# Optimization experiments

Hardware: AMD Instinct MI355X
Metric: run time of the kernel (lower is better)

The kernel has to match this reference:

```python
import jax, jax.numpy as jnp
import numpy as np

D_MODEL = 512
N_HEADS = 8
D_HEAD = D_MODEL // N_HEADS


def entmax15(z, axis=-1):
    """Exact sort-based entmax-1.5 along `axis` (Peters et al. 2019)."""
    z = jnp.moveaxis(z, axis, -1)
    x = z / 2.0
    x = x - jnp.max(x, axis=-1, keepdims=True)
    x_srt = -jnp.sort(-x, axis=-1)  # descending
    D = x_srt.shape[-1]
    k = jnp.arange(1, D + 1, dtype=x.dtype)
    cs = jnp.cumsum(x_srt, axis=-1)
    cs2 = jnp.cumsum(x_srt * x_srt, axis=-1)
    mean = cs / k
    ss = k * (cs2 / k - mean * mean)
    delta = (1.0 - ss) / k
    tau = mean - jnp.sqrt(jnp.clip(delta, 0.0))
    support = (tau <= x_srt).astype(jnp.int32)
    support_size = jnp.sum(support, axis=-1, keepdims=True)  # >= 1
    tau_star = jnp.take_along_axis(tau, support_size - 1, axis=-1)
    out = jnp.square(jnp.clip(x - tau_star, 0.0))
    return jnp.moveaxis(out, -1, axis)


def setup_inputs() -> dict:
    key = jax.random.key(0)
    ks = jax.random.split(key, 12)
    B, L = 8, 1024
    s = 1.0 / np.sqrt(D_MODEL)
    inp = {
        "query": jax.random.normal(ks[0], (B, L, D_MODEL), jnp.float32),
        "key": jax.random.normal(ks[1], (B, L, D_MODEL), jnp.float32),
        "value": jax.random.normal(ks[2], (B, L, D_MODEL), jnp.float32),
        "key_padding_mask": jnp.zeros((B, L), jnp.bool_),
        "q_w": jax.random.uniform(ks[3], (D_MODEL, D_MODEL), jnp.float32, -s, s),
        "q_b": jax.random.uniform(ks[4], (D_MODEL,), jnp.float32, -s, s),
        "k_w": jax.random.uniform(ks[5], (D_MODEL, D_MODEL), jnp.float32, -s, s),
        "k_b": jax.random.uniform(ks[6], (D_MODEL,), jnp.float32, -s, s),
        "v_w": jax.random.uniform(ks[7], (D_MODEL, D_MODEL), jnp.float32, -s, s),
        "v_b": jax.random.uniform(ks[8], (D_MODEL,), jnp.float32, -s, s),
        "out_w": jax.random.uniform(ks[9], (D_MODEL, D_MODEL), jnp.float32, -s, s),
        "out_b": jax.random.uniform(ks[10], (D_MODEL,), jnp.float32, -s, s),
    }
    return inp


def reference(query, key, value, key_padding_mask, q_w, q_b, k_w, k_b, v_w, v_b, out_w, out_b):
    B, L, _ = query.shape
    scale = D_HEAD ** -0.5
    # torch Linear: y = x @ W^T + b
    def split_heads(x):
        return x.reshape(B, L, N_HEADS, D_HEAD).transpose(0, 2, 1, 3)  # [B,H,L,d]
    q = split_heads(query @ q_w.T + q_b)
    k = split_heads(key @ k_w.T + k_b)
    v = split_heads(value @ v_w.T + v_b)
    scores = jnp.einsum('bhqd,bhkd->bhqk', q, k) * scale  # [B,H,L,L]
    mask = key_padding_mask[:, None, None, :]
    scores = jnp.where(mask, jnp.asarray(-1e9, scores.dtype), scores)
    attn = entmax15(scores, axis=-1)  # dropout in eval mode -> identity
    ctx = jnp.einsum('bhqk,bhkd->bhqd', attn, v)
    ctx = ctx.transpose(0, 2, 1, 3).reshape(B, L, D_MODEL)
    return ctx @ out_w.T + out_b
```

## Files before the change

### kernel.cpp

```cpp
#include <hip/hip_runtime.h>
#include <stdint.h>

typedef _Float16 f16;
typedef __attribute__((ext_vector_type(8))) f16 f16x8;
typedef __attribute__((ext_vector_type(2))) f16 h2;
typedef __attribute__((ext_vector_type(4))) float f32x4;
typedef unsigned short u16;
typedef unsigned int u32;
typedef unsigned char u8;

#define LL 1024
#define DM 512

__device__ __forceinline__ u16 f2h(float f){ return __builtin_bit_cast(u16, (f16)f); }
__device__ __forceinline__ u32 pack2(float a, float b){
  h2 v; v.x = (f16)a; v.y = (f16)b; return __builtin_bit_cast(u32, v);
}
__device__ __forceinline__ f32x4 mfma16h(f16x8 a, f16x8 b, f32x4 c){
  return __builtin_amdgcn_mfma_f32_16x16x32_f16(a, b, c, 0, 0, 0);
}

template<int CTRL>
__device__ __forceinline__ float dpp_mov(float x){
  return __builtin_bit_cast(float,
    __builtin_amdgcn_update_dpp(0, __builtin_bit_cast(int, x), CTRL, 0xF, 0xF, true));
}
__device__ __forceinline__ float red_add16(float v){
  v += dpp_mov<0x128>(v);
  v += dpp_mov<0x124>(v);
  v += dpp_mov<0x122>(v);
  v += dpp_mov<0x121>(v);
  return v;
}
__device__ __forceinline__ float red_max16(float v){
  v = fmaxf(v, dpp_mov<0x128>(v));
  v = fmaxf(v, dpp_mov<0x124>(v));
  v = fmaxf(v, dpp_mov<0x122>(v));
  v = fmaxf(v, dpp_mov<0x121>(v));
  return v;
}
__device__ __forceinline__ float red_add32(float v){
  v = red_add16(v);
  v += __shfl_xor(v, 16);
  return v;
}
__device__ __forceinline__ float red_max32(float v){
  v = red_max16(v);
  v = fmaxf(v, __shfl_xor(v, 16));
  return v;
}

struct CvtArgs {
  const float* src[7];
  u16* dst[7];
  int n4[7];
};

__global__ __launch_bounds__(256) void cvt_kernel(CvtArgs a){
  int seg = blockIdx.y;
  const float4* s = (const float4*)a.src[seg];
  ushort4* d = (ushort4*)a.dst[seg];
  int n4 = a.n4[seg];
  for (int i = blockIdx.x*blockDim.x + threadIdx.x; i < n4; i += gridDim.x*blockDim.x){
    float4 v = s[i];
    ushort4 o;
    o.x = f2h(v.x); o.y = f2h(v.y); o.z = f2h(v.z); o.w = f2h(v.w);
    d[i] = o;
  }
}

struct QkvArgs {
  const u16* A[3];
  const u16* W[3];
  const float* bias[3];
  u16* dst[3];
  float scale[3];
};

__global__ __launch_bounds__(256,2) void proj_qkv(QkvArgs args){
  __shared__ u16 SM[128*128];
  u16* As = SM;
  u16* Bs = SM + 128*64;
  const int tid = threadIdx.x;
  const int w = tid>>6, lane = tid&63;
  const int g = lane>>4, r16 = lane&15;
  const int wr = w>>1, wc = w&1;

  const int which = blockIdx.y>>2, nt = blockIdx.y&3;
  const bool isV = (which==2);
  const u16* A = args.A[which];
  const u16* W = args.W[which];
  const float* bias = args.bias[which];
  u16* dsth = args.dst[which];
  const float scale = args.scale[which];

  const int m0 = blockIdx.x*128, n0 = nt*128;

  f32x4 acc[4][4] = {};

  int rowc[4], slc[4];
  #pragma unroll
  for (int i=0;i<4;++i){
    int c = i*256+tid;
    rowc[i] = c>>3;
    slc[i] = (c&7) ^ ((c>>3)&7);
  }

  const int fswz = r16 & 7;

  for (int k0=0; k0<DM; k0+=64){
    #pragma unroll
    for (int i=0;i<4;++i){
      int c = i*256+tid;
      __builtin_amdgcn_global_load_lds(
        (const __attribute__((address_space(1))) void*)(A + (size_t)(m0+rowc[i])*DM + k0 + slc[i]*8),
        (__attribute__((address_space(3))) void*)(&As[c*8]), 16, 0, 0);
      __builtin_amdgcn_global_load_lds(
        (const __attribute__((address_space(1))) void*)(W + (size_t)(n0+rowc[i])*DM + k0 + slc[i]*8),
        (__attribute__((address_space(3))) void*)(&Bs[c*8]), 16, 0, 0);
    }
    __syncthreads();

    f16x8 af[4][2], bfr[4][2];
    #pragma unroll
    for (int mi=0; mi<4; ++mi){
      int row = wr*64 + mi*16 + r16;
      #pragma unroll
      for (int ks=0; ks<2; ++ks)
        af[mi][ks] = *(const f16x8*)(&As[row*64 + ((ks*4+g)^fswz)*8]);
    }
    #pragma unroll
    for (int ni=0; ni<4; ++ni){
      int row = wc*64 + ni*16 + r16;
      #pragma unroll
      for (int ks=0; ks<2; ++ks)
        bfr[ni][ks] = *(const f16x8*)(&Bs[row*64 + ((ks*4+g)^fswz)*8]);
    }
    if (isV){
      #pragma unroll
      for (int mi=0; mi<4; ++mi)
        #pragma unroll
        for (int ni=0; ni<4; ++ni){
          acc[mi][ni] = mfma16h(af[mi][0], bfr[ni][0], acc[mi][ni]);
          acc[mi][ni] = mfma16h(af[mi][1], bfr[ni][1], acc[mi][ni]);
        }
    } else {
      #pragma unroll
      for (int mi=0; mi<4; ++mi)
        #pragma unroll
        for (int ni=0; ni<4; ++ni){
          acc[mi][ni] = mfma16h(bfr[ni][0], af[mi][0], acc[mi][ni]);
          acc[mi][ni] = mfma16h(bfr[ni][1], af[mi][1], acc[mi][ni]);
        }
    }
    __syncthreads();
  }

  if (!isV){
    #pragma unroll
    for (int mi=0; mi<4; ++mi){
      #pragma unroll
      for (int ni=0; ni<4; ++ni){
        f32x4 a = acc[mi][ni];
        int row = wr*64 + mi*16 + r16;
        int c   = wc*16 + ni*4 + g;
        float4 bv = *(const float4*)(bias + n0 + c*4);
        uint2 pk;
        pk.x = pack2((a[0]+bv.x)*scale, (a[1]+bv.y)*scale);
        pk.y = pack2((a[2]+bv.z)*scale, (a[3]+bv.w)*scale);
        *(uint2*)(&SM[row*128 + ((c ^ ((row&7)<<2))<<2)]) = pk;
      }
    }
  } else {
    #pragma unroll
    for (int mi=0; mi<4; ++mi){
      #pragma unroll
      for (int ni=0; ni<4; ++ni){
        f32x4 a = acc[mi][ni];
        int fl = wc*64 + ni*16 + r16;
        int kc = wr*16 + mi*4 + g;
        float bv = bias[n0 + fl];
        uint2 pk;
        pk.x = pack2(a[0]+bv, a[1]+bv);
        pk.y = pack2(a[2]+bv, a[3]+bv);
        *(uint2*)(&SM[fl*128 + ((kc ^ ((fl&7)<<2))<<2)]) = pk;
      }
    }
  }
  __syncthreads();

  #pragma unroll
  for (int rr=0; rr<8; ++rr){
    int row = w*32 + rr*4 + (lane>>4);
    int c0 = (lane&15)*2;
    int cs = c0 ^ ((row&7)<<2);
    uint4 v = *(const uint4*)(&SM[row*128 + (cs<<2)]);
    if (!isV){
      *(uint4*)(dsth + (size_t)(m0+row)*DM + n0 + (c0<<2)) = v;
    } else {
      int n = n0 + row;
      int hh = n>>6, d = n&63, bb = m0>>10;
      *(uint4*)(dsth + (size_t)((bb*8+hh)*64 + d)*1024 + (m0&1023) + (c0<<2)) = v;
    }
  }
}

__global__ __launch_bounds__(256,2) void proj_out(
    const u16* __restrict__ A, const u16* __restrict__ W,
    const float* __restrict__ bias, float* __restrict__ dstf)
{
  __shared__ u16 As[64*64];
  __shared__ u16 Bs[128*64];
  const int tid = threadIdx.x;
  const int w = tid>>6, lane = tid&63;
  const int g = lane>>4, r16 = lane&15;
  const int m0 = blockIdx.x*64, n0 = blockIdx.y*128;

  f32x4 acc[4][2] = {};

  int rowa[2], slota[2];
  #pragma unroll
  for (int i=0;i<2;++i){ int c = i*256+tid; rowa[i]=c>>3; slota[i]=c&7; }
  int rowb[4], slotb[4];
  #pragma unroll
  for (int i=0;i<4;++i){ int c = i*256+tid; rowb[i]=c>>3; slotb[i]=c&7; }

  uint4 ra[2], rb[4];
  #pragma unroll
  for (int i=0;i<2;++i)
    ra[i] = *(const uint4*)(A + (size_t)(m0+rowa[i])*DM + slota[i]*8);
  #pragma unroll
  for (int i=0;i<4;++i)
    rb[i] = *(const uint4*)(W + (size_t)(n0+rowb[i])*DM + slotb[i]*8);

  const int fswz = r16 & 7;

  for (int k0=0; k0<DM; k0+=64){
    __syncthreads();
    #pragma unroll
    for (int i=0;i<2;++i)
      *(uint4*)(&As[rowa[i]*64 + (slota[i]^(rowa[i]&7))*8]) = ra[i];
    #pragma unroll
    for (int i=0;i<4;++i)
      *(uint4*)(&Bs[rowb[i]*64 + (slotb[i]^(rowb[i]&7))*8]) = rb[i];
    __syncthreads();
    int kn = (k0+64 < DM) ? (k0+64) : 0;
    #pragma unroll
    for (int i=0;i<2;++i)
      ra[i] = *(const uint4*)(A + (size_t)(m0+rowa[i])*DM + kn + slota[i]*8);
    #pragma unroll
    for (int i=0;i<4;++i)
      rb[i] = *(const uint4*)(W + (size_t)(n0+rowb[i])*DM + kn + slotb[i]*8);

    f16x8 af[4][2], bfr[2][2];
    #pragma unroll
    for (int mi=0; mi<4; ++mi){
      int row = mi*16 + r16;
      #pragma unroll
      for (int ks=0; ks<2; ++ks)
        af[mi][ks] = *(const f16x8*)(&As[row*64 + ((ks*4+g)^fswz)*8]);
    }
    #pragma unroll
    for (int ni=0; ni<2; ++ni){
      int row = w*32 + ni*16 + r16;
      #pragma unroll
      for (int ks=0; ks<2; ++ks)
        bfr[ni][ks] = *(const f16x8*)(&Bs[row*64 + ((ks*4+g)^fswz)*8]);
    }
    #pragma unroll
    for (int mi=0; mi<4; ++mi)
      #pragma unroll
      for (int ni=0; ni<2; ++ni){
        acc[mi][ni] = mfma16h(bfr[ni][0], af[mi][0], acc[mi][ni]);
        acc[mi][ni] = mfma16h(bfr[ni][1], af[mi][1], acc[mi][ni]);
      }
  }

  #pragma unroll
  for (int mi=0; mi<4; ++mi){
    #pragma unroll
    for (int ni=0; ni<2; ++ni){
      int m  = m0 + mi*16 + r16;
      int nb = n0 + w*32 + ni*16 + g*4;
      float4 bv = *(const float4*)(bias + nb);
      float4 o;
      o.x = acc[mi][ni][0]+bv.x; o.y = acc[mi][ni][1]+bv.y;
      o.z = acc[mi][ni][2]+bv.z; o.w = acc[mi][ni][3]+bv.w;
      *(float4*)(dstf + (size_t)m*DM + nb) = o;
    }
  }
}

__global__ __launch_bounds__(1024,8) void attn_entmax(
    const u16* __restrict__ Qf, const u16* __restrict__ Kf,
    const u16* __restrict__ Vt, const u8* __restrict__ mask,
    u16* __restrict__ ctx)
{
  __shared__ u16 S[32*1024];
  __shared__ float P2[2048];

  const int tid = threadIdx.x, w = tid>>6, lane = tid&63;
  const int g = lane>>4, r16 = lane&15;
  const int bid = blockIdx.x;
  const int bh = ((bid&7)<<3) | ((bid>>3)&7);
  const int qb = bid>>6;
  const int b = bh>>3, h = bh&7;
  const int q0 = qb*32;
  const u16* Qb = Qf + ((size_t)(b*LL + q0))*DM + h*64;
  const u16* Kb = Kf + ((size_t)(b*LL))*DM + h*64;

  f16x8 qf[2][2];
  #pragma unroll
  for (int qi=0;qi<2;++qi){
    qf[qi][0] = *(const f16x8*)(Qb + (size_t)(qi*16 + r16)*DM + g*8);
    qf[qi][1] = *(const f16x8*)(Qb + (size_t)(qi*16 + r16)*DM + 32 + g*8);
  }
  {
    f16x8 kc0, kc1, kn0, kn1;
    {
      const u16* kp = Kb + (size_t)(w*64 + r16)*DM + g*8;
      kc0 = *(const f16x8*)(kp);
      kc1 = *(const f16x8*)(kp + 32);
    }
    #pragma unroll
    for (int kt=0; kt<4; ++kt){
      if (kt < 3){
        const u16* kp = Kb + (size_t)(w*64 + (kt+1)*16 + r16)*DM + g*8;
        kn0 = *(const f16x8*)(kp);
        kn1 = *(const f16x8*)(kp + 32);
      }
      int kb = w*64 + kt*16 + g*4;
      u32 m4 = *(const u32*)(mask + b*LL + kb);
      #pragma unroll
      for (int qi=0; qi<2; ++qi){
        f32x4 acc = {};
        acc = mfma16h(kc0, qf[qi][0], acc);
        acc = mfma16h(kc1, qf[qi][1], acc);
        float v0 = (m4 & 0xFFu)       ? -30000.f : acc[0];
        float v1 = (m4 & 0xFF00u)     ? -30000.f : acc[1];
        float v2 = (m4 & 0xFF0000u)   ? -30000.f : acc[2];
        float v3 = (m4 & 0xFF000000u) ? -30000.f : acc[3];
        int row = qi*16 + r16;
        int cc = ((kb>>6)&7) ^ (row&7);
        uint2 pk; pk.x = pack2(v0,v1); pk.y = pack2(v2,v3);
        *(uint2*)(&S[row*LL + (kb ^ (cc<<3))]) = pk;
      }
      kc0 = kn0; kc1 = kn1;
    }
  }
  __syncthreads();

  {
    const int row = w*2 + (lane>>5);
    const int l32 = lane&31;
    int offs[4];
    h2 zp[16];
    #pragma unroll
    for (int c=0;c<4;++c){
      int kb = l32*32 + c*8;
      int cc = ((kb>>6)&7) ^ (row&7);
      offs[c] = row*LL + (kb ^ (cc<<3));
      uint4 v = *(const uint4*)(&S[offs[c]]);
      zp[c*4+0] = __builtin_bit_cast(h2, v.x);
      zp[c*4+1] = __builtin_bit_cast(h2, v.y);
      zp[c*4+2] = __builtin_bit_cast(h2, v.z);
      zp[c*4+3] = __builtin_bit_cast(h2, v.w);
    }
    h2 m2 = zp[0];
    #pragma unroll
    for (int t=1;t<16;++t) m2 = __builtin_elementwise_max(m2, zp[t]);
    float mx = red_max32(fmaxf((float)m2.x, (float)m2.y));

    const h2 zero2 = (h2)(f16)0;
    float lo = mx - 1.0f, hi = mx, tau = mx - 0.5f;
    #pragma unroll 1
    for (int it=0; it<6; ++it){
      f16 th = (f16)tau;
      h2 t2; t2.x = th; t2.y = th;
      h2 s1a = zero2, s1b = zero2, s2a = zero2, s2b = zero2;
      #pragma unroll
      for (int t=0;t<16;t+=2){
        h2 d0 = __builtin_elementwise_max(zp[t]   - t2, zero2);
        h2 d1 = __builtin_elementwise_max(zp[t+1] - t2, zero2);
        s1a = s1a + d0;        s1b = s1b + d1;
        s2a = s2a + d0*d0;     s2b = s2b + d1*d1;
      }
      h2 s1h = s1a + s1b, s2h = s2a + s2b;
      float s1 = red_add32((float)s1h.x + (float)s1h.y);
      float s2 = red_add32((float)s2h.x + (float)s2h.y);
      if (s2 >= 1.0f) lo = tau; else hi = tau;
      float tn = tau + (s2 - 1.0f)/(2.0f*s1);
      tau = (tn >= lo && tn < hi) ? tn : 0.5f*(lo+hi);
    }

    {
      f16 th = (f16)tau;
      h2 t2; t2.x = th; t2.y = th;
      h2 psa = zero2, psb = zero2;
      #pragma unroll
      for (int t=0;t<16;t+=2){
        h2 d0 = __builtin_elementwise_max(zp[t]   - t2, zero2);
        h2 d1 = __builtin_elementwise_max(zp[t+1] - t2, zero2);
        h2 p0 = d0*d0, p1 = d1*d1;
        zp[t] = p0; zp[t+1] = p1;
        psa = psa + p0; psb = psb + p1;
      }
      h2 ps2 = psa + psb;
      float ps = red_add32((float)ps2.x + (float)ps2.y);
      f16 iv = (f16)(1.0f/ps);
      h2 i2; i2.x = iv; i2.y = iv;
      #pragma unroll
      for (int c=0;c<4;++c){
        uint4 v;
        v.x = __builtin_bit_cast(u32, (h2)(zp[c*4+0]*i2));
        v.y = __builtin_bit_cast(u32, (h2)(zp[c*4+1]*i2));
        v.z = __builtin_bit_cast(u32, (h2)(zp[c*4+2]*i2));
        v.w = __builtin_bit_cast(u32, (h2)(zp[c*4+3]*i2));
        *(uint4*)(&S[offs[c]]) = v;
      }
    }
  }
  __syncthreads();

  const int qi = w>>3, di = (w>>1)&3, kh = w&1;
  const u16* vrow = Vt + (size_t)(bh*64 + di*16 + r16)*LL;
  const int prow = qi*16 + r16;
  f32x4 o0 = {}, o1 = {};
  {
    f16x8 pc0, pc1, vc0, vc1, pn0, pn1, vn0, vn1;
    const int base = kh*16;
    {
      int k0c = (base+0)*32 + g*8;
      int k1c = (base+1)*32 + g*8;
      int cc0 = ((k0c>>6)&7) ^ (prow&7);
      int cc1 = ((k1c>>6)&7) ^ (prow&7);
      pc0 = *(const f16x8*)(&S[prow*LL + (k0c ^ (cc0<<3))]);
      vc0 = *(const f16x8*)(vrow + k0c);
      pc1 = *(const f16x8*)(&S[prow*LL + (k1c ^ (cc1<<3))]);
      vc1 = *(const f16x8*)(vrow + k1c);
    }
    #pragma unroll
    for (int grp=0; grp<8; ++grp){
      if (grp < 7){
        int k0n = (base+grp*2+2)*32 + g*8;
        int k1n = (base+grp*2+3)*32 + g*8;
        int cc0 = ((k0n>>6)&7) ^ (prow&7);
        int cc1 = ((k1n>>6)&7) ^ (prow&7);
        pn0 = *(const f16x8*)(&S[prow*LL + (k0n ^ (cc0<<3))]);
        vn0 = *(const f16x8*)(vrow + k0n);
        pn1 = *(const f16x8*)(&S[prow*LL + (k1n ^ (cc1<<3))]);
        vn1 = *(const f16x8*)(vrow + k1n);
      }
      o0 = mfma16h(pc0, vc0, o0);
      o1 = mfma16h(pc1, vc1, o1);
      pc0 = pn0; vc0 = vn0; pc1 = pn1; vc1 = vn1;
    }
  }
  const int pair = qi*4 + di;
  if (kh == 1){
    float4 o;
    o.x = o0[0]+o1[0]; o.y = o0[1]+o1[1]; o.z = o0[2]+o1[2]; o.w = o0[3]+o1[3];
    *(float4*)(&P2[pair*256 + r16*16 + g*4]) = o;
  }
  __syncthreads();
  if (kh == 0){
    float4 p = *(const float4*)(&P2[pair*256 + r16*16 + g*4]);
    u16* cp = ctx + (size_t)(b*LL + q0 + qi*16 + g*4)*DM + h*64 + di*16 + r16;
    cp[0*DM] = f2h(o0[0]+o1[0]+p.x);
    cp[1*DM] = f2h(o0[1]+o1[1]+p.y);
    cp[2*DM] = f2h(o0[2]+o1[2]+p.z);
    cp[3*DM] = f2h(o0[3]+o1[3]+p.w);
  }
}

extern "C" void kernel_launch(void* const* d_in, const int* in_sizes, int n_in,
                              void* d_out, int out_size, void* d_ws, size_t ws_size,
                              hipStream_t stream) {
  const float* query = (const float*)d_in[0];
  const float* key   = (const float*)d_in[1];
  const float* value = (const float*)d_in[2];
  const u8*    maskp = (const u8*)d_in[3];
  const float* q_w = (const float*)d_in[4];
  const float* q_b = (const float*)d_in[5];
  const float* k_w = (const float*)d_in[6];
  const float* k_b = (const float*)d_in[7];
  const float* v_w = (const float*)d_in[8];
  const float* v_b = (const float*)d_in[9];
  const float* out_w = (const float*)d_in[10];
  const float* out_b = (const float*)d_in[11];
  float* out = (float*)d_out;

  u16* qx = (u16*)d_ws;
  u16* kx = qx + 4194304;
  u16* vx = kx + 4194304;
  u16* wq = vx + 4194304;
  u16* wk = wq + 262144;
  u16* wv = wk + 262144;
  u16* wo = wv + 262144;
  u16* Qbuf = wo + 262144;
  u16* Kbuf = Qbuf + 4194304;
  u16* Vt   = Kbuf + 4194304;
  u16* ctxb = Vt + 4194304;

  CvtArgs ca;
  ca.src[0]=query; ca.dst[0]=qx; ca.n4[0]=8*LL*DM/4;
  ca.src[1]=key;   ca.dst[1]=kx; ca.n4[1]=8*LL*DM/4;
  ca.src[2]=value; ca.dst[2]=vx; ca.n4[2]=8*LL*DM/4;
  ca.src[3]=q_w;   ca.dst[3]=wq; ca.n4[3]=DM*DM/4;
  ca.src[4]=k_w;   ca.dst[4]=wk; ca.n4[4]=DM*DM/4;
  ca.src[5]=v_w;   ca.dst[5]=wv; ca.n4[5]=DM*DM/4;
  ca.src[6]=out_w; ca.dst[6]=wo; ca.n4[6]=DM*DM/4;
  cvt_kernel<<<dim3(512,7),256,0,stream>>>(ca);

  QkvArgs qa;
  qa.A[0]=qx; qa.A[1]=kx; qa.A[2]=vx;
  qa.W[0]=wq; qa.W[1]=wk; qa.W[2]=wv;
  qa.bias[0]=q_b; qa.bias[1]=k_b; qa.bias[2]=v_b;
  qa.dst[0]=Qbuf; qa.dst[1]=Kbuf; qa.dst[2]=Vt;
  qa.scale[0]=0.0625f; qa.scale[1]=1.0f; qa.scale[2]=1.0f;

  proj_qkv<<<dim3(64,12),256,0,stream>>>(qa);

  attn_entmax<<<dim3(2048),1024,0,stream>>>(Qbuf, Kbuf, Vt, maskp, ctxb);

  proj_out<<<dim3(128,4),256,0,stream>>>(ctxb, wo, out_b, out);
}
```

Measured before the change: 186.2 us.

## Halve attention block to 8 waves and software-pipeline QK/entmax/PV over two row halves

The attention kernel now runs 512 threads instead of 1024 and splits its 32 query rows into two 16-row halves. Score computation, entmax normalisation and the PV matmul are staggered across the halves, with odd and even waves doing the phases in opposite order so MFMA work and VALU/reduction work from different waves can overlap. s_setprio is raised around the PV MFMA loop, and the split-K partial buffer is double-buffered so the first half's output store overlaps the second half's PV. Each wave now does twice the work, and the kernel adds an extra barrier and changes occupancy through the new launch bounds.

```diff
diff --git a/kernel.cpp b/kernel.cpp
--- a/kernel.cpp
+++ b/kernel.cpp
@@ -291,13 +291,14 @@
   }
 }
 
-__global__ __launch_bounds__(1024,8) void attn_entmax(
+__global__ __launch_bounds__(512,4) void attn_entmax(
     const u16* __restrict__ Qf, const u16* __restrict__ Kf,
     const u16* __restrict__ Vt, const u8* __restrict__ mask,
     u16* __restrict__ ctx)
 {
   __shared__ u16 S[32*1024];
-  __shared__ float P2[2048];
+  __shared__ float P2a[1024];
+  __shared__ float P2b[1024];
 
   const int tid = threadIdx.x, w = tid>>6, lane = tid&63;
   const int g = lane>>4, r16 = lane&15;
@@ -308,6 +309,7 @@
   const int q0 = qb*32;
   const u16* Qb = Qf + ((size_t)(b*LL + q0))*DM + h*64;
   const u16* Kb = Kf + ((size_t)(b*LL))*DM + h*64;
+  const int di = w&3, kh = w>>2;
 
   f16x8 qf[2][2];
   #pragma unroll
@@ -315,43 +317,32 @@
     qf[qi][0] = *(const f16x8*)(Qb + (size_t)(qi*16 + r16)*DM + g*8);
     qf[qi][1] = *(const f16x8*)(Qb + (size_t)(qi*16 + r16)*DM + 32 + g*8);
   }
-  {
-    f16x8 kc0, kc1, kn0, kn1;
-    {
-      const u16* kp = Kb + (size_t)(w*64 + r16)*DM + g*8;
-      kc0 = *(const f16x8*)(kp);
-      kc1 = *(const f16x8*)(kp + 32);
-    }
-    #pragma unroll
-    for (int kt=0; kt<4; ++kt){
-      if (kt < 3){
-        const u16* kp = Kb + (size_t)(w*64 + (kt+1)*16 + r16)*DM + g*8;
-        kn0 = *(const f16x8*)(kp);
-        kn1 = *(const f16x8*)(kp + 32);
-      }
-      int kb = w*64 + kt*16 + g*4;
+
+  auto phaseA = [&](int hf){
+    #pragma unroll
+    for (int kt=0; kt<8; ++kt){
+      int krow = w*128 + kt*16;
+      const u16* kp = Kb + (size_t)(krow + r16)*DM + g*8;
+      f16x8 kf0 = *(const f16x8*)(kp);
+      f16x8 kf1 = *(const f16x8*)(kp + 32);
+      int kb = krow + g*4;
       u32 m4 = *(const u32*)(mask + b*LL + kb);
-      #pragma unroll
-      for (int qi=0; qi<2; ++qi){
-        f32x4 acc = {};
-        acc = mfma16h(kc0, qf[qi][0], acc);
-        acc = mfma16h(kc1, qf[qi][1], acc);
-        float v0 = (m4 & 0xFFu)       ? -30000.f : acc[0];
-        float v1 = (m4 & 0xFF00u)     ? -30000.f : acc[1];
-        float v2 = (m4 & 0xFF0000u)   ? -30000.f : acc[2];
-        float v3 = (m4 & 0xFF000000u) ? -30000.f : acc[3];
-        int row = qi*16 + r16;
-        int cc = ((kb>>6)&7) ^ (row&7);
-        uint2 pk; pk.x = pack2(v0,v1); pk.y = pack2(v2,v3);
-        *(uint2*)(&S[row*LL + (kb ^ (cc<<3))]) = pk;
-      }
-      kc0 = kn0; kc1 = kn1;
-    }
-  }
-  __syncthreads();
-
-  {
-    const int row = w*2 + (lane>>5);
+      f32x4 acc = {};
+      acc = mfma16h(kf0, qf[hf][0], acc);
+      acc = mfma16h(kf1, qf[hf][1], acc);
+      float v0 = (m4 & 0xFFu)       ? -30000.f : acc[0];
+      float v1 = (m4 & 0xFF00u)     ? -30000.f : acc[1];
+      float v2 = (m4 & 0xFF0000u)   ? -30000.f : acc[2];
+      float v3 = (m4 & 0xFF000000u) ? -30000.f : acc[3];
+      int row = hf*16 + r16;
+      int cc = ((kb>>6)&7) ^ (row&7);
+      uint2 pk; pk.x = pack2(v0,v1); pk.y = pack2(v2,v3);
+      *(uint2*)(&S[row*LL + (kb ^ (cc<<3))]) = pk;
+    }
+  };
+
+  auto phaseB = [&](int hf){
+    const int row = hf*16 + w*2 + (lane>>5);
     const int l32 = lane&31;
     int offs[4];
     h2 zp[16];
@@ -392,7 +383,6 @@
       float tn = tau + (s2 - 1.0f)/(2.0f*s1);
       tau = (tn >= lo && tn < hi) ? tn : 0.5f*(lo+hi);
     }
-
     {
       f16 th = (f16)tau;
       h2 t2; t2.x = th; t2.y = th;
@@ -419,16 +409,13 @@
         *(uint4*)(&S[offs[c]]) = v;
       }
     }
-  }
-  __syncthreads();
-
-  const int qi = w>>3, di = (w>>1)&3, kh = w&1;
-  const u16* vrow = Vt + (size_t)(bh*64 + di*16 + r16)*LL;
-  const int prow = qi*16 + r16;
-  f32x4 o0 = {}, o1 = {};
-  {
+  };
+
+  auto phaseC = [&](int hf, f32x4& o0, f32x4& o1, float* P2x){
+    const u16* vrow = Vt + (size_t)(bh*64 + di*16 + r16)*LL;
+    const int prow = hf*16 + r16;
+    const int base = kh*16;
     f16x8 pc0, pc1, vc0, vc1, pn0, pn1, vn0, vn1;
-    const int base = kh*16;
     {
       int k0c = (base+0)*32 + g*8;
       int k1c = (base+1)*32 + g*8;
@@ -439,6 +426,7 @@
       pc1 = *(const f16x8*)(&S[prow*LL + (k1c ^ (cc1<<3))]);
       vc1 = *(const f16x8*)(vrow + k1c);
     }
+    __builtin_amdgcn_s_setprio(1);
     #pragma unroll
     for (int grp=0; grp<8; ++grp){
       if (grp < 7){
@@ -455,22 +443,41 @@
       o1 = mfma16h(pc1, vc1, o1);
       pc0 = pn0; vc0 = vn0; pc1 = pn1; vc1 = vn1;
     }
-  }
-  const int pair = qi*4 + di;
-  if (kh == 1){
-    float4 o;
-    o.x = o0[0]+o1[0]; o.y = o0[1]+o1[1]; o.z = o0[2]+o1[2]; o.w = o0[3]+o1[3];
-    *(float4*)(&P2[pair*256 + r16*16 + g*4]) = o;
-  }
-  __syncthreads();
-  if (kh == 0){
-    float4 p = *(const float4*)(&P2[pair*256 + r16*16 + g*4]);
-    u16* cp = ctx + (size_t)(b*LL + q0 + qi*16 + g*4)*DM + h*64 + di*16 + r16;
+    __builtin_amdgcn_s_setprio(0);
+    if (kh == 1){
+      float4 o;
+      o.x = o0[0]+o1[0]; o.y = o0[1]+o1[1]; o.z = o0[2]+o1[2]; o.w = o0[3]+o1[3];
+      *(float4*)(&P2x[di*256 + r16*16 + g*4]) = o;
+    }
+  };
+
+  auto mergeStore = [&](int hf, f32x4 o0, f32x4 o1, const float* P2x){
+    float4 p = *(const float4*)(&P2x[di*256 + r16*16 + g*4]);
+    u16* cp = ctx + (size_t)(b*LL + q0 + hf*16 + g*4)*DM + h*64 + di*16 + r16;
     cp[0*DM] = f2h(o0[0]+o1[0]+p.x);
     cp[1*DM] = f2h(o0[1]+o1[1]+p.y);
     cp[2*DM] = f2h(o0[2]+o1[2]+p.z);
     cp[3*DM] = f2h(o0[3]+o1[3]+p.w);
-  }
+  };
+
+  phaseA(0);
+  __syncthreads();
+
+  if (w & 1){ phaseA(1); phaseB(0); }
+  else      { phaseB(0); phaseA(1); }
+  __syncthreads();
+
+  f32x4 c0o0 = {}, c0o1 = {};
+  if (w & 1){ phaseB(1); phaseC(0, c0o0, c0o1, P2a); }
+  else      { phaseC(0, c0o0, c0o1, P2a); phaseB(1); }
+  __syncthreads();
+
+  f32x4 c1o0 = {}, c1o1 = {};
+  if (kh == 0) mergeStore(0, c0o0, c0o1, P2a);
+  phaseC(1, c1o0, c1o1, P2b);
+  __syncthreads();
+
+  if (kh == 0) mergeStore(1, c1o0, c1o1, P2b);
 }
 
 extern "C" void kernel_launch(void* const* d_in, const int* in_sizes, int n_in,
@@ -521,7 +528,7 @@
 
   proj_qkv<<<dim3(64,12),256,0,stream>>>(qa);
 
-  attn_entmax<<<dim3(2048),1024,0,stream>>>(Qbuf, Kbuf, Vt, maskp, ctxb);
+  attn_entmax<<<dim3(2048),512,0,stream>>>(Qbuf, Kbuf, Vt, maskp, ctxb);
 
   proj_out<<<dim3(128,4),256,0,stream>>>(ctxb, wo, out_b, out);
 }
```

Result: slower. 199.7 us (+7.2%).
